# Kernel tuning notes

Measured on AMD Instinct MI355X. Metric: run time of the kernel, lower is better.

## Reference

```python
import jax, jax.numpy as jnp
import numpy as np
import math

CHANNEL = 512
NUM_HEAD = 8
HEAD_DIM = 64


def setup_inputs() -> dict:
    key = jax.random.key(0)
    ks = jax.random.split(key, 9)
    d = NUM_HEAD * HEAD_DIM  # 512
    s = 1.0 / math.sqrt(CHANNEL)
    return {
        "x": jax.random.normal(ks[0], (8, CHANNEL, 32, 32), dtype=jnp.float32),
        "wq": jax.random.normal(ks[1], (CHANNEL, d), dtype=jnp.float32) * s,
        "bq": jnp.zeros((d,), dtype=jnp.float32),
        "wk": jax.random.normal(ks[2], (CHANNEL, d), dtype=jnp.float32) * s,
        "bk": jnp.zeros((d,), dtype=jnp.float32),
        "wv": jax.random.normal(ks[3], (CHANNEL, d), dtype=jnp.float32) * s,
        "bv": jnp.zeros((d,), dtype=jnp.float32),
        "wo": jax.random.normal(ks[4], (d, CHANNEL), dtype=jnp.float32) * s,
        "bo": jnp.zeros((CHANNEL,), dtype=jnp.float32),
    }


def reference(x, wq, bq, wk, bk, wv, bv, wo, bo):
    B, C, H, W = x.shape
    S = H * W
    # [B, C, H, W] -> [B, S, C]
    xr = x.transpose(0, 2, 3, 1).reshape(B, S, C)
    q = (xr @ wq + bq).reshape(B, S, NUM_HEAD, HEAD_DIM)
    k = (xr @ wk + bk).reshape(B, S, NUM_HEAD, HEAD_DIM)
    v = (xr @ wv + bv).reshape(B, S, NUM_HEAD, HEAD_DIM)
    # NOTE: original scales by 1/sqrt(channel), not 1/sqrt(head_dim)
    energy = jnp.einsum('bqhd,bkhd->bhqk', q, k) / math.sqrt(C)
    attn = jax.nn.softmax(energy, axis=-1)
    out = jnp.einsum('bhqk,bkhd->bqhd', attn, v).reshape(B, S, NUM_HEAD * HEAD_DIM)
    out = out @ wo + bo  # [B, S, C]
    out = out.transpose(0, 2, 1).reshape(B, C, H, W)
    return x + out
```

## Files before the change

### kernel.cpp

```cpp
#include <hip/hip_runtime.h>
#include <hip/hip_bf16.h>

typedef __bf16 bf16_t;
typedef __attribute__((ext_vector_type(8))) __bf16 bf16x8;
typedef __attribute__((ext_vector_type(4))) __bf16 bf16x4;
typedef __attribute__((ext_vector_type(4))) float f32x4;

#define AS1 __attribute__((address_space(1)))
#define AS3 __attribute__((address_space(3)))

__device__ __forceinline__ void gload_lds16(const void* g, void* l) {
  __builtin_amdgcn_global_load_lds((const AS1 void*)g, (AS3 void*)l, 16, 0, 0);
}

__global__ void __launch_bounds__(256) prep_kernel(
    const float* __restrict__ x, const float* __restrict__ w0,
    const float* __restrict__ w1, const float* __restrict__ w2,
    const float* __restrict__ w3, bf16_t* __restrict__ xr, bf16_t* __restrict__ t0,
    bf16_t* __restrict__ t1, bf16_t* __restrict__ t2, bf16_t* __restrict__ t3) {
  __shared__ float tile[32][33];
  const int tx = threadIdx.x, ty = threadIdx.y;
  int t = blockIdx.x;
  const float* src;
  bf16_t* dst;
  int ld_src, ld_dst, r0, c0;
  if (t < 1024) {
    int z = t >> 8, rem = t & 255;
    src = (z == 0) ? w0 : (z == 1) ? w1 : (z == 2) ? w2 : w3;
    dst = (z == 0) ? t0 : (z == 1) ? t1 : (z == 2) ? t2 : t3;
    ld_src = 512; ld_dst = 512;
    r0 = (rem & 15) * 32; c0 = (rem >> 4) * 32;
  } else {
    t -= 1024;
    int b = t >> 9, rem = t & 511;
    src = x + (size_t)b * 512 * 1024;
    dst = xr + (size_t)b * 1024 * 512;
    ld_src = 1024; ld_dst = 512;
    r0 = (rem & 15) * 32; c0 = (rem >> 4) * 32;
  }
#pragma unroll
  for (int i = 0; i < 32; i += 8)
    tile[ty + i][tx] = src[(r0 + ty + i) * ld_src + c0 + tx];
  __syncthreads();
#pragma unroll
  for (int i = 0; i < 32; i += 8)
    dst[(c0 + ty + i) * ld_dst + r0 + tx] = (bf16_t)tile[tx][ty + i];
}

__device__ __forceinline__ void gemm_nt_128x128_p4(const bf16_t* __restrict__ Abase,
                                                   const bf16_t* __restrict__ Bbase,
                                                   bf16_t (*As)[128 * 32],
                                                   bf16_t (*Bs)[128 * 32],
                                                   f32x4 acc[4][4]) {
  const int tid = threadIdx.x;
  const int lane = tid & 63;
  const int wid = tid >> 6;
  const int wr = wid >> 1, wc = wid & 1;
  const int lrow = lane & 15;
  const int kgrp = lane >> 4;
  const int r0 = tid >> 2;
  const int cb = (tid & 3) * 16;

#pragma unroll
  for (int p = 0; p < 2; ++p) {
    const int kt = p * 32;
#pragma unroll
    for (int j = 0; j < 2; ++j) {
      int row = j * 64 + r0;
      gload_lds16((const char*)(Abase + row * 512 + kt) + cb, (char*)As[p] + row * 64 + cb);
    }
#pragma unroll
    for (int j = 0; j < 2; ++j) {
      int row = j * 64 + r0;
      gload_lds16((const char*)(Bbase + row * 512 + kt) + cb, (char*)Bs[p] + row * 64 + cb);
    }
  }

  for (int t = 0; t < 16; ++t) {
    const int cur = t & 3;
    if (t < 14) {
      const int nxt = (t + 2) & 3;
      const int kt = (t + 2) * 32;
#pragma unroll
      for (int j = 0; j < 2; ++j) {
        int row = j * 64 + r0;
        gload_lds16((const char*)(Abase + row * 512 + kt) + cb,
                    (char*)As[nxt] + row * 64 + cb);
      }
#pragma unroll
      for (int j = 0; j < 2; ++j) {
        int row = j * 64 + r0;
        gload_lds16((const char*)(Bbase + row * 512 + kt) + cb,
                    (char*)Bs[nxt] + row * 64 + cb);
      }
      asm volatile("s_waitcnt vmcnt(8)" ::: "memory");
    } else if (t == 14) {
      asm volatile("s_waitcnt vmcnt(4)" ::: "memory");
    } else {
      asm volatile("s_waitcnt vmcnt(0)" ::: "memory");
    }
    __builtin_amdgcn_sched_barrier(0);
    __builtin_amdgcn_s_barrier();

    bf16x8 a[4], b[4];
#pragma unroll
    for (int mf = 0; mf < 4; ++mf)
      a[mf] = *(const bf16x8*)(As[cur] + (wr * 64 + mf * 16 + lrow) * 32 + kgrp * 8);
#pragma unroll
    for (int nf = 0; nf < 4; ++nf)
      b[nf] = *(const bf16x8*)(Bs[cur] + (wc * 64 + nf * 16 + lrow) * 32 + kgrp * 8);
    __builtin_amdgcn_s_setprio(1);
#pragma unroll
    for (int mf = 0; mf < 4; ++mf)
#pragma unroll
      for (int nf = 0; nf < 4; ++nf)
        acc[mf][nf] = __builtin_amdgcn_mfma_f32_16x16x32_bf16(a[mf], b[nf], acc[mf][nf], 0, 0, 0);
    __builtin_amdgcn_s_setprio(0);
  }
}

__device__ __forceinline__ void gemm_nt_128x256_p3(const bf16_t* __restrict__ Abase,
                                                   const bf16_t* __restrict__ Bbase,
                                                   bf16_t (*As)[128 * 32],
                                                   bf16_t (*Bs)[256 * 32],
                                                   f32x4 acc[4][8]) {
  const int tid = threadIdx.x;
  const int lane = tid & 63;
  const int wid = tid >> 6;
  const int wr = wid >> 1, wc = wid & 1;
  const int lrow = lane & 15;
  const int kgrp = lane >> 4;
  const int r0 = tid >> 2;
  const int cb = (tid & 3) * 16;

#pragma unroll
  for (int p = 0; p < 2; ++p) {
    const int kt = p * 32;
#pragma unroll
    for (int j = 0; j < 2; ++j) {
      int row = j * 64 + r0;
      gload_lds16((const char*)(Abase + row * 512 + kt) + cb, (char*)As[p] + row * 64 + cb);
    }
#pragma unroll
    for (int j = 0; j < 4; ++j) {
      int row = j * 64 + r0;
      gload_lds16((const char*)(Bbase + row * 512 + kt) + cb, (char*)Bs[p] + row * 64 + cb);
    }
  }
  asm volatile("s_waitcnt vmcnt(6)" ::: "memory");
  __builtin_amdgcn_sched_barrier(0);

  int cur = 0, nxt = 2;
  for (int t = 0; t < 16; ++t) {
    __builtin_amdgcn_s_barrier();
    __builtin_amdgcn_sched_barrier(0);
    if (t < 14) {
      const int kt = (t + 2) * 32;
#pragma unroll
      for (int j = 0; j < 2; ++j) {
        int row = j * 64 + r0;
        gload_lds16((const char*)(Abase + row * 512 + kt) + cb,
                    (char*)As[nxt] + row * 64 + cb);
      }
#pragma unroll
      for (int j = 0; j < 4; ++j) {
        int row = j * 64 + r0;
        gload_lds16((const char*)(Bbase + row * 512 + kt) + cb,
                    (char*)Bs[nxt] + row * 64 + cb);
      }
    }

    bf16x8 a[4], b[8];
#pragma unroll
    for (int mf = 0; mf < 4; ++mf)
      a[mf] = *(const bf16x8*)(As[cur] + (wr * 64 + mf * 16 + lrow) * 32 + kgrp * 8);
#pragma unroll
    for (int nf = 0; nf < 8; ++nf)
      b[nf] = *(const bf16x8*)(Bs[cur] + (wc * 128 + nf * 16 + lrow) * 32 + kgrp * 8);
    __builtin_amdgcn_s_setprio(1);
#pragma unroll
    for (int mf = 0; mf < 4; ++mf)
#pragma unroll
      for (int nf = 0; nf < 8; ++nf)
        acc[mf][nf] = __builtin_amdgcn_mfma_f32_16x16x32_bf16(a[mf], b[nf], acc[mf][nf], 0, 0, 0);
    __builtin_amdgcn_s_setprio(0);
    if (t < 14) {
      asm volatile("s_waitcnt vmcnt(6)" ::: "memory");
    } else {
      asm volatile("s_waitcnt vmcnt(0)" ::: "memory");
    }
    __builtin_amdgcn_sched_barrier(0);
    cur = (cur == 2) ? 0 : cur + 1;
    nxt = (nxt == 2) ? 0 : nxt + 1;
  }
}

__global__ void __launch_bounds__(256, 2) gemm_qkv_kernel(
    const bf16_t* __restrict__ xr, const bf16_t* __restrict__ wT ,
    const float* __restrict__ bq, const float* __restrict__ bk,
    const float* __restrict__ bv, bf16_t* __restrict__ qo, bf16_t* __restrict__ ko,
    bf16_t* __restrict__ vto) {
  __shared__ bf16_t As[3][128 * 32];
  __shared__ bf16_t Bs[3][256 * 32];
  const int bn = blockIdx.x, bm = blockIdx.y;
  const int z = bn >> 1;
  const float* bias = (z == 0) ? bq : (z == 1) ? bk : bv;
  f32x4 acc[4][8] = {};
  gemm_nt_128x256_p3(xr + bm * 128 * 512, wT + (size_t)bn * 256 * 512, As, Bs, acc);
  const int lane = threadIdx.x & 63, wid = threadIdx.x >> 6;
  const int lrow = lane & 15, kgrp = lane >> 4;
  const int wr = wid >> 1, wc = wid & 1;
  const int row0 = bm * 128 + wr * 64;
  const int col0 = bn * 256 + wc * 128;
  const float qscale = 0.044194173824159216f * 1.4426950408889634f;
  if (z == 2) {
#pragma unroll
    for (int mf = 0; mf < 4; ++mf)
#pragma unroll
      for (int nf = 0; nf < 8; ++nf) {
        int nl = (col0 + nf * 16 + lrow) & 511;
        int h = nl >> 6, d = nl & 63;
        float bb = bias[nl];
        int m0 = row0 + mf * 16 + kgrp * 4;
        int b = m0 >> 10, s = m0 & 1023;
        bf16x4 pk;
#pragma unroll
        for (int r = 0; r < 4; ++r) pk[r] = (bf16_t)(acc[mf][nf][r] + bb);
        *(bf16x4*)(vto + (((size_t)(b * 8 + h) * 64 + d) * 1024 + s)) = pk;
      }
  } else {
    bf16_t* out = (z == 0) ? qo : ko;
    const float sc = (z == 0) ? qscale : 1.0f;
#pragma unroll
    for (int mf = 0; mf < 4; ++mf)
#pragma unroll
      for (int nf = 0; nf < 8; ++nf) {
        int nl = (col0 + nf * 16 + lrow) & 511;
        int h = nl >> 6, d = nl & 63;
        float bb = bias[nl];
#pragma unroll
        for (int r = 0; r < 4; ++r) {
          int m = row0 + mf * 16 + kgrp * 4 + r;
          int b = m >> 10, s = m & 1023;
          out[((b * 8 + h) * 1024 + s) * 64 + d] = (bf16_t)((acc[mf][nf][r] + bb) * sc);
        }
      }
  }
}

__global__ void __launch_bounds__(256, 2) attn_kernel(const bf16_t* __restrict__ q,
                                                      const bf16_t* __restrict__ k,
                                                      const bf16_t* __restrict__ vt,
                                                      bf16_t* __restrict__ attn_out) {
  __shared__ char Ks[4][8192];
  __shared__ char Vs[4][8192];
  __shared__ char Ps[4][4096];
  const int tid = threadIdx.x;
  const int lane = tid & 63, wid = tid >> 6;
  const int lrow = lane & 15, kgrp = lane >> 4;
  const int bh = blockIdx.x, qb = blockIdx.y;
  const int b = bh >> 3, h = bh & 7;

  const char* khb = (const char*)(k + (size_t)bh * 1024 * 64);
  const char* vthb = (const char*)(vt + (size_t)bh * 64 * 1024);
  const bf16_t* qh = q + (size_t)bh * 1024 * 64;

  const int qbase = qb * 128 + wid * 32;
  bf16x8 qa[2][2];
#pragma unroll
  for (int qf = 0; qf < 2; ++qf) {
    int qrow = qbase + qf * 16 + lrow;
    qa[qf][0] = *(const bf16x8*)(qh + qrow * 64 + kgrp * 8);
    qa[qf][1] = *(const bf16x8*)(qh + qrow * 64 + 32 + kgrp * 8);
  }

  char* Pw = Ps[wid];
  const int srow = tid >> 3;
  const int sc2 = tid & 7;

  float l_part[2] = {0.f, 0.f};
  f32x4 o[2][4] = {};

#pragma unroll
  for (int p = 0; p < 2; ++p) {
    const char* kg = khb + p * (64 * 128);
    const char* vg = vthb + p * 128;
#pragma unroll
    for (int j = 0; j < 2; ++j) {
      int row = j * 32 + srow;
      gload_lds16(kg + row * 128 + ((sc2 ^ (row & 7)) * 16), Ks[p] + j * 4096 + tid * 16);
    }
#pragma unroll
    for (int j = 0; j < 2; ++j) {
      int row = j * 32 + srow;
      gload_lds16(vg + row * 2048 + ((sc2 ^ (row & 7)) * 16), Vs[p] + j * 4096 + tid * 16);
    }
  }

  for (int t = 0; t < 16; ++t) {
    const int cur = t & 3;
    if (t < 14) {
      const int nxt = (t + 2) & 3;
      const char* kg = khb + (t + 2) * (64 * 128);
      const char* vg = vthb + (t + 2) * 128;
#pragma unroll
      for (int j = 0; j < 2; ++j) {
        int row = j * 32 + srow;
        gload_lds16(kg + row * 128 + ((sc2 ^ (row & 7)) * 16),
                    Ks[nxt] + j * 4096 + tid * 16);
      }
#pragma unroll
      for (int j = 0; j < 2; ++j) {
        int row = j * 32 + srow;
        gload_lds16(vg + row * 2048 + ((sc2 ^ (row & 7)) * 16),
                    Vs[nxt] + j * 4096 + tid * 16);
      }
      asm volatile("s_waitcnt vmcnt(8)" ::: "memory");
    } else if (t == 14) {
      asm volatile("s_waitcnt vmcnt(4)" ::: "memory");
    } else {
      asm volatile("s_waitcnt vmcnt(0)" ::: "memory");
    }
    __builtin_amdgcn_sched_barrier(0);
    __builtin_amdgcn_s_barrier();

    const char* Kc = Ks[cur];
    const char* Vc = Vs[cur];

    f32x4 sa[2][4] = {};
    __builtin_amdgcn_s_setprio(1);
#pragma unroll
    for (int c = 0; c < 4; ++c) {
      int krow = c * 16 + lrow;
      bf16x8 k0 = *(const bf16x8*)(Kc + krow * 128 + ((kgrp ^ (krow & 7)) * 16));
      bf16x8 k1 = *(const bf16x8*)(Kc + krow * 128 + (((4 + kgrp) ^ (krow & 7)) * 16));
#pragma unroll
      for (int qf = 0; qf < 2; ++qf) {
        sa[qf][c] = __builtin_amdgcn_mfma_f32_16x16x32_bf16(k0, qa[qf][0], sa[qf][c], 0, 0, 0);
        sa[qf][c] = __builtin_amdgcn_mfma_f32_16x16x32_bf16(k1, qa[qf][1], sa[qf][c], 0, 0, 0);
      }
    }
    __builtin_amdgcn_s_setprio(0);

#pragma unroll
    for (int qf = 0; qf < 2; ++qf) {
      int prow = qf * 16 + lrow;
      float rs = 0.f;
#pragma unroll
      for (int c = 0; c < 4; ++c) {
        bf16x4 pk;
#pragma unroll
        for (int r = 0; r < 4; ++r) {
          float p = exp2f(sa[qf][c][r]);
          rs += p;
          pk[r] = (bf16_t)p;
        }
        int chunk = (c * 2 + (kgrp >> 1)) ^ (prow & 7);
        *(bf16x4*)(Pw + prow * 128 + chunk * 16 + (kgrp & 1) * 8) = pk;
      }
      l_part[qf] += rs;
    }

    __builtin_amdgcn_s_setprio(1);
#pragma unroll
    for (int kk = 0; kk < 2; ++kk) {
      bf16x8 pa[2];
#pragma unroll
      for (int qf = 0; qf < 2; ++qf) {
        int prow = qf * 16 + lrow;
        int pchunk = (kk * 4 + kgrp) ^ (prow & 7);
        pa[qf] = *(const bf16x8*)(Pw + prow * 128 + pchunk * 16);
      }
#pragma unroll
      for (int nfo = 0; nfo < 4; ++nfo) {
        int vrow = nfo * 16 + lrow;
        int vchunk = (kk * 4 + kgrp) ^ (vrow & 7);
        bf16x8 vb = *(const bf16x8*)(Vc + vrow * 128 + vchunk * 16);
#pragma unroll
        for (int qf = 0; qf < 2; ++qf)
          o[qf][nfo] = __builtin_amdgcn_mfma_f32_16x16x32_bf16(pa[qf], vb, o[qf][nfo], 0, 0, 0);
      }
    }
    __builtin_amdgcn_s_setprio(0);
  }

#pragma unroll
  for (int qf = 0; qf < 2; ++qf) {
    l_part[qf] += __shfl_xor(l_part[qf], 16, 64);
    l_part[qf] += __shfl_xor(l_part[qf], 32, 64);
  }
#pragma unroll
  for (int qf = 0; qf < 2; ++qf)
#pragma unroll
    for (int r = 0; r < 4; ++r) {
      float inv = 1.0f / __shfl(l_part[qf], kgrp * 4 + r, 64);
      int s = qbase + qf * 16 + kgrp * 4 + r;
#pragma unroll
      for (int nfo = 0; nfo < 4; ++nfo) {
        int d = nfo * 16 + lrow;
        attn_out[((b * 1024 + s) * 8 + h) * 64 + d] = (bf16_t)(o[qf][nfo][r] * inv);
      }
    }
}

__global__ void __launch_bounds__(256, 2) gemm_out_kernel(const bf16_t* __restrict__ woT,
                                                          const bf16_t* __restrict__ attn,
                                                          const float* __restrict__ x,
                                                          const float* __restrict__ bo,
                                                          float* __restrict__ out) {
  __shared__ bf16_t As[4][128 * 32];
  __shared__ bf16_t Bs[4][128 * 32];
  const int bn = blockIdx.x, bm = blockIdx.y;
  f32x4 acc[4][4] = {};
  gemm_nt_128x128_p4(woT + bm * 128 * 512, attn + bn * 128 * 512, As, Bs, acc);
  const int lane = threadIdx.x & 63, wid = threadIdx.x >> 6;
  const int wr = wid >> 1, wc = wid & 1;
  const int c0 = bm * 128 + wr * 64;
  const int s0g = bn * 128 + wc * 64;
#pragma unroll
  for (int mf = 0; mf < 4; ++mf)
#pragma unroll
    for (int r = 0; r < 4; ++r) {
      int c = c0 + mf * 16 + (lane >> 4) * 4 + r;
      float bias = bo[c];
#pragma unroll
      for (int nf = 0; nf < 4; ++nf) {
        int n = s0g + nf * 16 + (lane & 15);
        int b = n >> 10, s = n & 1023;
        int idx = (b * 512 + c) * 1024 + s;
        out[idx] = x[idx] + acc[mf][nf][r] + bias;
      }
    }
}

extern "C" void kernel_launch(void* const* d_in, const int* in_sizes, int n_in,
                              void* d_out, int out_size, void* d_ws, size_t ws_size,
                              hipStream_t stream) {
  const float* x  = (const float*)d_in[0];
  const float* wq = (const float*)d_in[1];
  const float* bq = (const float*)d_in[2];
  const float* wk = (const float*)d_in[3];
  const float* bk = (const float*)d_in[4];
  const float* wv = (const float*)d_in[5];
  const float* bv = (const float*)d_in[6];
  const float* wo = (const float*)d_in[7];
  const float* bo = (const float*)d_in[8];
  float* out = (float*)d_out;

  char* ws = (char*)d_ws;
  const size_t SZ_XR = (size_t)8192 * 512 * 2;
  const size_t SZ_W  = (size_t)512 * 512 * 2;
  const size_t SZ_T  = (size_t)8 * 8 * 1024 * 64 * 2;
  bf16_t* xr   = (bf16_t*)(ws);
  bf16_t* wqT  = (bf16_t*)(ws + SZ_XR);
  bf16_t* wkT  = (bf16_t*)(ws + SZ_XR + SZ_W);
  bf16_t* wvT  = (bf16_t*)(ws + SZ_XR + 2 * SZ_W);
  bf16_t* woT  = (bf16_t*)(ws + SZ_XR + 3 * SZ_W);
  bf16_t* qd   = (bf16_t*)(ws + SZ_XR + 4 * SZ_W);
  bf16_t* kd   = (bf16_t*)(ws + SZ_XR + 4 * SZ_W + SZ_T);
  bf16_t* vtd  = (bf16_t*)(ws + SZ_XR + 4 * SZ_W + 2 * SZ_T);
  bf16_t* attn = (bf16_t*)(ws);

  prep_kernel<<<dim3(5120), dim3(32, 8), 0, stream>>>(x, wq, wk, wv, wo, xr, wqT, wkT,
                                                      wvT, woT);
  gemm_qkv_kernel<<<dim3(6, 64), 256, 0, stream>>>(xr, wqT, bq, bk, bv, qd, kd, vtd);
  attn_kernel<<<dim3(64, 8), 256, 0, stream>>>(qd, kd, vtd, attn);
  gemm_out_kernel<<<dim3(64, 4), 256, 0, stream>>>(woT, attn, x, bo, out);
}
```

Before: 85.26 us.

## Widen attention blocks to 512 threads and vectorize prep transpose with 64x64 tiles

The attention kernel now runs 8 waves per block covering 256 query rows, so each K/V tile loaded into LDS is shared by twice as many waves. The pipeline moves from 4-deep to 3-stage buffering with a single 16-byte load per thread per tile, and the wait and barrier are reordered to sit at the end and start of each iteration. The prep transpose kernel switches to 64x64 tiles with float4 reads and 8-wide bf16 writes, cutting the block count fourfold. Doubling the block size halves the attention grid to 256 blocks and lowers occupancy to one block per CU, which may reduce latency hiding.

New measurement: 86.56 us. No clear change (+1.5%).

```diff
diff --git a/kernel.cpp b/kernel.cpp
--- a/kernel.cpp
+++ b/kernel.cpp
@@ -18,33 +18,50 @@
     const float* __restrict__ w1, const float* __restrict__ w2,
     const float* __restrict__ w3, bf16_t* __restrict__ xr, bf16_t* __restrict__ t0,
     bf16_t* __restrict__ t1, bf16_t* __restrict__ t2, bf16_t* __restrict__ t3) {
-  __shared__ float tile[32][33];
-  const int tx = threadIdx.x, ty = threadIdx.y;
+  __shared__ float tile[64][69];
   int t = blockIdx.x;
   const float* src;
   bf16_t* dst;
-  int ld_src, ld_dst, r0, c0;
-  if (t < 1024) {
-    int z = t >> 8, rem = t & 255;
+  int ld_src, ld_dst, R0, C0;
+  if (t < 256) {
+    int z = t >> 6, rem = t & 63;
     src = (z == 0) ? w0 : (z == 1) ? w1 : (z == 2) ? w2 : w3;
     dst = (z == 0) ? t0 : (z == 1) ? t1 : (z == 2) ? t2 : t3;
     ld_src = 512; ld_dst = 512;
-    r0 = (rem & 15) * 32; c0 = (rem >> 4) * 32;
+    R0 = (rem >> 3) * 64;
+    C0 = (rem & 7) * 64;
   } else {
-    t -= 1024;
-    int b = t >> 9, rem = t & 511;
+    t -= 256;
+    int b = t >> 7, rem = t & 127;
     src = x + (size_t)b * 512 * 1024;
     dst = xr + (size_t)b * 1024 * 512;
     ld_src = 1024; ld_dst = 512;
-    r0 = (rem & 15) * 32; c0 = (rem >> 4) * 32;
-  }
-#pragma unroll
-  for (int i = 0; i < 32; i += 8)
-    tile[ty + i][tx] = src[(r0 + ty + i) * ld_src + c0 + tx];
+    R0 = (rem >> 4) * 64;
+    C0 = (rem & 15) * 64;
+  }
+  const int tid = threadIdx.x;
+  const int rl = tid >> 4;
+  const int cl = (tid & 15) * 4;
+#pragma unroll
+  for (int p = 0; p < 4; ++p) {
+    int r = p * 16 + rl;
+    float4 v = *(const float4*)(src + (size_t)(R0 + r) * ld_src + C0 + cl);
+    tile[r][cl + 0] = v.x;
+    tile[r][cl + 1] = v.y;
+    tile[r][cl + 2] = v.z;
+    tile[r][cl + 3] = v.w;
+  }
   __syncthreads();
-#pragma unroll
-  for (int i = 0; i < 32; i += 8)
-    dst[(c0 + ty + i) * ld_dst + r0 + tx] = (bf16_t)tile[tx][ty + i];
+  const int kk = tid & 7;
+  const int cw = tid >> 3;
+#pragma unroll
+  for (int p = 0; p < 2; ++p) {
+    int c = p * 32 + cw;
+    bf16x8 o;
+#pragma unroll
+    for (int j = 0; j < 8; ++j) o[j] = (bf16_t)tile[kk * 8 + j][c];
+    *(bf16x8*)(dst + (size_t)(C0 + c) * ld_dst + R0 + kk * 8) = o;
+  }
 }
 
 __device__ __forceinline__ void gemm_nt_128x128_p4(const bf16_t* __restrict__ Abase,
@@ -248,13 +265,13 @@
   }
 }
 
-__global__ void __launch_bounds__(256, 2) attn_kernel(const bf16_t* __restrict__ q,
+__global__ void __launch_bounds__(512, 1) attn_kernel(const bf16_t* __restrict__ q,
                                                       const bf16_t* __restrict__ k,
                                                       const bf16_t* __restrict__ vt,
                                                       bf16_t* __restrict__ attn_out) {
-  __shared__ char Ks[4][8192];
-  __shared__ char Vs[4][8192];
-  __shared__ char Ps[4][4096];
+  __shared__ char Ks[3][8192];
+  __shared__ char Vs[3][8192];
+  __shared__ char Ps[8][4096];
   const int tid = threadIdx.x;
   const int lane = tid & 63, wid = tid >> 6;
   const int lrow = lane & 15, kgrp = lane >> 4;
@@ -265,7 +282,7 @@
   const char* vthb = (const char*)(vt + (size_t)bh * 64 * 1024);
   const bf16_t* qh = q + (size_t)bh * 1024 * 64;
 
-  const int qbase = qb * 128 + wid * 32;
+  const int qbase = qb * 256 + wid * 32;
   bf16x8 qa[2][2];
 #pragma unroll
   for (int qf = 0; qf < 2; ++qf) {
@@ -283,46 +300,24 @@
 
 #pragma unroll
   for (int p = 0; p < 2; ++p) {
-    const char* kg = khb + p * (64 * 128);
-    const char* vg = vthb + p * 128;
-#pragma unroll
-    for (int j = 0; j < 2; ++j) {
-      int row = j * 32 + srow;
-      gload_lds16(kg + row * 128 + ((sc2 ^ (row & 7)) * 16), Ks[p] + j * 4096 + tid * 16);
-    }
-#pragma unroll
-    for (int j = 0; j < 2; ++j) {
-      int row = j * 32 + srow;
-      gload_lds16(vg + row * 2048 + ((sc2 ^ (row & 7)) * 16), Vs[p] + j * 4096 + tid * 16);
-    }
-  }
-
+    gload_lds16(khb + p * 8192 + srow * 128 + ((sc2 ^ (srow & 7)) * 16),
+                Ks[p] + tid * 16);
+    gload_lds16(vthb + p * 128 + srow * 2048 + ((sc2 ^ (srow & 7)) * 16),
+                Vs[p] + tid * 16);
+  }
+  asm volatile("s_waitcnt vmcnt(2)" ::: "memory");
+  __builtin_amdgcn_sched_barrier(0);
+
+  int cur = 0, nxt = 2;
   for (int t = 0; t < 16; ++t) {
-    const int cur = t & 3;
+    __builtin_amdgcn_s_barrier();
+    __builtin_amdgcn_sched_barrier(0);
     if (t < 14) {
-      const int nxt = (t + 2) & 3;
-      const char* kg = khb + (t + 2) * (64 * 128);
-      const char* vg = vthb + (t + 2) * 128;
-#pragma unroll
-      for (int j = 0; j < 2; ++j) {
-        int row = j * 32 + srow;
-        gload_lds16(kg + row * 128 + ((sc2 ^ (row & 7)) * 16),
-                    Ks[nxt] + j * 4096 + tid * 16);
-      }
-#pragma unroll
-      for (int j = 0; j < 2; ++j) {
-        int row = j * 32 + srow;
-        gload_lds16(vg + row * 2048 + ((sc2 ^ (row & 7)) * 16),
-                    Vs[nxt] + j * 4096 + tid * 16);
-      }
-      asm volatile("s_waitcnt vmcnt(8)" ::: "memory");
-    } else if (t == 14) {
-      asm volatile("s_waitcnt vmcnt(4)" ::: "memory");
-    } else {
-      asm volatile("s_waitcnt vmcnt(0)" ::: "memory");
-    }
-    __builtin_amdgcn_sched_barrier(0);
-    __builtin_amdgcn_s_barrier();
+      gload_lds16(khb + (t + 2) * 8192 + srow * 128 + ((sc2 ^ (srow & 7)) * 16),
+                  Ks[nxt] + tid * 16);
+      gload_lds16(vthb + (t + 2) * 128 + srow * 2048 + ((sc2 ^ (srow & 7)) * 16),
+                  Vs[nxt] + tid * 16);
+    }
 
     const char* Kc = Ks[cur];
     const char* Vc = Vs[cur];
@@ -382,6 +377,15 @@
       }
     }
     __builtin_amdgcn_s_setprio(0);
+
+    if (t < 14) {
+      asm volatile("s_waitcnt vmcnt(2)" ::: "memory");
+    } else {
+      asm volatile("s_waitcnt vmcnt(0)" ::: "memory");
+    }
+    __builtin_amdgcn_sched_barrier(0);
+    cur = (cur == 2) ? 0 : cur + 1;
+    nxt = (nxt == 2) ? 0 : nxt + 1;
   }
 
 #pragma unroll
@@ -461,9 +465,8 @@
   bf16_t* vtd  = (bf16_t*)(ws + SZ_XR + 4 * SZ_W + 2 * SZ_T);
   bf16_t* attn = (bf16_t*)(ws);
 
-  prep_kernel<<<dim3(5120), dim3(32, 8), 0, stream>>>(x, wq, wk, wv, wo, xr, wqT, wkT,
-                                                      wvT, woT);
+  prep_kernel<<<dim3(1280), 256, 0, stream>>>(x, wq, wk, wv, wo, xr, wqT, wkT, wvT, woT);
   gemm_qkv_kernel<<<dim3(6, 64), 256, 0, stream>>>(xr, wqT, bq, bk, bv, qd, kd, vtd);
-  attn_kernel<<<dim3(64, 8), 256, 0, stream>>>(qd, kd, vtd, attn);
+  attn_kernel<<<dim3(64, 4), 512, 0, stream>>>(qd, kd, vtd, attn);
   gemm_out_kernel<<<dim3(64, 4), 256, 0, stream>>>(woT, attn, x, bo, out);
 }
```
